# Optimization experiments

Hardware: AMD Instinct MI355X
Metric: run time of the kernel (lower is better)

Reference implementation:

```python
import jax, jax.numpy as jnp
import numpy as np
import math

D_MODEL = 1024
NUM_HEADS = 16
SEQ = 2048
BATCH = 4


def setup_inputs() -> dict:
    key = jax.random.key(0)
    ks = jax.random.split(key, 7)
    s = 0.02
    return {
        "x": jax.random.normal(ks[0], (BATCH, SEQ, D_MODEL), jnp.float32),
        "Wq": jax.random.normal(ks[1], (D_MODEL, D_MODEL), jnp.float32) * s,
        "bq": jax.random.normal(ks[2], (D_MODEL,), jnp.float32) * s,
        "Wkv": jax.random.normal(ks[3], (D_MODEL, 2 * D_MODEL), jnp.float32) * s,
        "bkv": jax.random.normal(ks[4], (2 * D_MODEL,), jnp.float32) * s,
        "Wo": jax.random.normal(ks[5], (D_MODEL, D_MODEL), jnp.float32) * s,
        "bo": jax.random.normal(ks[6], (D_MODEL,), jnp.float32) * s,
        "decoderMask": 1,
    }


def reference(x, Wq, bq, Wkv, bkv, Wo, bo, decoderMask):
    B, S, D = x.shape
    H = NUM_HEADS
    dh = D // H
    q_ = x @ Wq + bq              # [B,S,D]
    kv_ = x @ Wkv + bkv           # [B,S,2D] (self-attention: m is None)
    # Faithful to source: concat [q_, kv_] then reshape into heads of 3*dh,
    # which interleaves Q/KV projection columns across heads.
    qkv = jnp.concatenate([q_, kv_], axis=-1)          # [B,S,3D]
    qkv = qkv.reshape(B, S, H, 3 * dh).transpose(0, 2, 1, 3)  # [B,H,S,3dh]
    q, k, v = jnp.split(qkv, 3, axis=-1)               # each [B,H,S,dh]
    scaled = jnp.einsum("bhqd,bhkd->bhqk", q, k) / math.sqrt(dh)
    if decoderMask:
        mask = jnp.triu(jnp.full((S, S), -jnp.inf, dtype=scaled.dtype), k=1)
        scaled = scaled + mask
    attn = jax.nn.softmax(scaled, axis=-1)
    vals = jnp.einsum("bhqk,bhkd->bhqd", attn, v)      # [B,H,S,dh]
    vals = vals.transpose(0, 2, 1, 3).reshape(B, S, D)
    return vals @ Wo + bo
```

## Files before the change

kernel.cpp:

```cpp
#include <hip/hip_runtime.h>
#include <cstddef>
#include <cstdint>

#define SEQ   2048
#define BATCH 4
#define DM    1024
#define NH    16
#define DH    64
#define ROWS  (BATCH*SEQ)
#define NC3   3072
#define SM_SCALE 0.18033688f

typedef unsigned short u16;
typedef __attribute__((ext_vector_type(8))) short bf16x8;
typedef __attribute__((ext_vector_type(2))) float f32x2;
typedef __attribute__((ext_vector_type(4))) float f32x4;
typedef __attribute__((ext_vector_type(16))) float f32x16;
typedef __attribute__((ext_vector_type(4))) unsigned u32x4;
typedef __attribute__((ext_vector_type(2))) unsigned u32x2;

union V16 { f32x16 v; f32x2 p[8]; };

__device__ __forceinline__ u16 f2b(float f) {
  union { float f; unsigned u; } v; v.f = f;
  unsigned r = v.u + 0x7fffu + ((v.u >> 16) & 1u);
  return (u16)(r >> 16);
}

__device__ __forceinline__ unsigned cvt_pk_bf16(float lo, float hi) {
  unsigned r;
  asm("v_cvt_pk_bf16_f32 %0, %1, %2" : "=v"(r) : "v"(lo), "v"(hi));
  return r;
}

__device__ __forceinline__ void plswap(unsigned& a, unsigned& b) {
  auto rr = __builtin_amdgcn_permlane32_swap((int)a, (int)b, false, false);
  a = (unsigned)rr[0];
  b = (unsigned)rr[1];
}

__device__ __forceinline__ float ex2(float x) { return __builtin_amdgcn_exp2f(x); }

__device__ __forceinline__ void gld16(const void* g, void* l) {
  __builtin_amdgcn_global_load_lds((const __attribute__((address_space(1))) void*)g,
                                   (__attribute__((address_space(3))) void*)l,
                                   16, 0, 0);
}

__global__ __launch_bounds__(256) void prep_tw_kernel(
    const float* __restrict__ x, const float* __restrict__ bq,
    const float* __restrict__ bkv, u16* __restrict__ xb, float* __restrict__ bc,
    const float* __restrict__ Wq, const float* __restrict__ Wkv,
    const float* __restrict__ Wo, u16* __restrict__ Wt)
{
  __shared__ float t_[32][33];
  const int tid = threadIdx.x;
  if (blockIdx.x < 8192) {
    int i = blockIdx.x * 256 + tid;
    int idx = i * 4;
    float4 v = *(const float4*)(x + idx);
    u32x2 pv;
    pv[0] = cvt_pk_bf16(v.x, v.y);
    pv[1] = cvt_pk_bf16(v.z, v.w);
    *(u32x2*)&xb[idx] = pv;
    if (i < NC3) bc[i] = (i < DM) ? bq[i] : bkv[i - DM];
  } else {
    const int bid = blockIdx.x - 8192;
    const int n0 = (bid & 127) * 32, k0 = (bid >> 7) * 32;
    const int xcol = tid & 31, yrow = tid >> 5;
    #pragma unroll
    for (int it = 0; it < 4; ++it) {
      int k = k0 + yrow + it * 8;
      int n = n0 + xcol;
      float v;
      if (n < DM)           v = Wq[k * DM + n];
      else if (n < NC3)     v = Wkv[k * (2 * DM) + (n - DM)];
      else                  v = Wo[k * DM + (n - NC3)];
      t_[yrow + it * 8][xcol] = v;
    }
    __syncthreads();
    #pragma unroll
    for (int it = 0; it < 4; ++it) {
      int n = n0 + yrow + it * 8;
      int k = k0 + xcol;
      Wt[(size_t)n * DM + k] = f2b(t_[xcol][yrow + it * 8]);
    }
  }
}

__global__ __launch_bounds__(512, 2) void gemm8_qkv(
    const u16* __restrict__ A, const u16* __restrict__ Bt,
    const float* __restrict__ bias, u16* __restrict__ C, u16* __restrict__ Vt)
{
  constexpr int K = 1024, N = NC3;
  constexpr int ASLOT = 16384;
  constexpr int BBASE = 32768;
  constexpr int BSLOT = 12288;
  __shared__ alignas(16) u16 lds_[57344];

  const int tid = threadIdx.x;
  const int lane = tid & 63, wid = tid >> 6;
  const int wr2 = wid >> 2, wc4 = wid & 3;
  const int l15 = lane & 15, lhi = lane >> 4;

  const int bid = blockIdx.x;
  const int xcd = bid & 7, t = bid >> 3;
  const int row0 = (xcd * 4 + (t & 3)) * 256;
  const int hh   = t >> 2;
  const int col0 = hh * 192;

  const int sr = tid >> 3;
  const int scg = ((tid & 7) ^ (sr & 7)) * 8;
  const u16* aSrc = A  + (size_t)(row0 + sr) * K + scg;
  const u16* bSrc = Bt + (size_t)(col0 + sr) * K + scg;
  const int dLin = tid * 8;

  auto stA = [&](int kt, int u) {
    gld16(aSrc + (size_t)(u * 64) * K + kt * 64,
          lds_ + (kt & 1) * ASLOT + u * 4096 + dLin);
  };
  auto stB = [&](int kt, int u) {
    gld16(bSrc + (size_t)(u * 64) * K + kt * 64,
          lds_ + BBASE + (kt & 1) * BSLOT + u * 4096 + dLin);
  };

  int csw[2];
  csw[0] = ((lhi)     ^ (l15 & 7)) * 8;
  csw[1] = ((4 + lhi) ^ (l15 & 7)) * 8;
  const int aBase = wr2 * 8192 + l15 * 64;
  const int bBase = BBASE + (wc4 * 48 + l15) * 64;

  f32x4 acc[8][3];
  #pragma unroll
  for (int m = 0; m < 8; ++m)
    #pragma unroll
    for (int n = 0; n < 3; ++n) { f32x4 z = {0.f, 0.f, 0.f, 0.f}; acc[m][n] = z; }

  stA(0, 0); stA(0, 1); stA(0, 2); stA(0, 3);
  stB(0, 0); stB(0, 1); stB(0, 2);
  stB(1, 0); stB(1, 1); stB(1, 2);
  asm volatile("s_waitcnt vmcnt(3)" ::: "memory");
  __builtin_amdgcn_s_barrier();

  constexpr int KT2 = K / 128;
  for (int j = 0; j < KT2; ++j) {
    const bool last = (j == KT2 - 1);
    #pragma unroll
    for (int hk = 0; hk < 2; ++hk) {
      const int slotA = hk * ASLOT;
      const int slotB = hk * BSLOT;
      bf16x8 bfr[3][2];
      #pragma unroll
      for (int ph = 0; ph < 4; ++ph) {
        const int gp = hk * 4 + ph;
        if (ph == 0) {
          #pragma unroll
          for (int n = 0; n < 3; ++n)
            #pragma unroll
            for (int kk = 0; kk < 2; ++kk)
              bfr[n][kk] = *(const bf16x8*)&lds_[bBase + slotB + n * 1024 + csw[kk]];
        }
        bf16x8 af[2][2];
        #pragma unroll
        for (int mi = 0; mi < 2; ++mi)
          #pragma unroll
          for (int kk = 0; kk < 2; ++kk)
            af[mi][kk] = *(const bf16x8*)&lds_[aBase + slotA + (ph * 2 + mi) * 1024 + csw[kk]];
        switch (gp) {
          case 0: stA(2 * j + 1, 0); stA(2 * j + 1, 1); break;
          case 1: stA(2 * j + 1, 2); stA(2 * j + 1, 3); break;
          case 2: if (!last) { stB(2 * j + 2, 0); stB(2 * j + 2, 1); } break;
          case 3: if (!last) { stB(2 * j + 2, 2); } break;
          case 4: if (!last) { stA(2 * j + 2, 0); stA(2 * j + 2, 1); } break;
          case 5: if (!last) { stA(2 * j + 2, 2); stA(2 * j + 2, 3); } break;
          case 6: if (!last) { stB(2 * j + 3, 0); stB(2 * j + 3, 1); } break;
          case 7: if (!last) { stB(2 * j + 3, 2); } break;
        }
        __builtin_amdgcn_s_barrier();
        asm volatile("s_waitcnt lgkmcnt(0)" ::: "memory");
        __builtin_amdgcn_sched_barrier(0);
        __builtin_amdgcn_s_setprio(1);
        #pragma unroll
        for (int mi = 0; mi < 2; ++mi)
          #pragma unroll
          for (int n = 0; n < 3; ++n) {
            acc[ph * 2 + mi][n] =
                __builtin_amdgcn_mfma_f32_16x16x32_bf16(af[mi][0], bfr[n][0], acc[ph * 2 + mi][n], 0, 0, 0);
            acc[ph * 2 + mi][n] =
                __builtin_amdgcn_mfma_f32_16x16x32_bf16(af[mi][1], bfr[n][1], acc[ph * 2 + mi][n], 0, 0, 0);
          }
        __builtin_amdgcn_s_setprio(0);
        if (gp == 3) {
          if (last) { asm volatile("s_waitcnt vmcnt(0)" ::: "memory"); }
          else      { asm volatile("s_waitcnt vmcnt(3)" ::: "memory"); }
        } else if (gp == 7 && !last) {
          asm volatile("s_waitcnt vmcnt(3)" ::: "memory");
        }
        __builtin_amdgcn_s_barrier();
      }
    }
  }

  #pragma unroll
  for (int m = 0; m < 8; ++m) {
    const int row = row0 + wr2 * 128 + m * 16 + lhi * 4;
    #pragma unroll
    for (int n = 0; n < 3; ++n) {
      const int cc  = wc4 * 48 + n * 16 + l15;
      const int col = col0 + cc;
      const float bv = bias[col];
      if (cc < 128) {
        const float qs = (cc < 64) ? SM_SCALE : 1.f;
        #pragma unroll
        for (int r = 0; r < 4; ++r)
          C[(size_t)(row + r) * N + col] = f2b((acc[m][n][r] + bv) * qs);
      } else {
        u16 wv[4];
        #pragma unroll
        for (int r = 0; r < 4; ++r) wv[r] = f2b(acc[m][n][r] + bv);
        const int bb = row >> 11, jj = row & (SEQ - 1);
        u16* vt = Vt + ((size_t)(bb * NH + hh) * 64 + (cc - 128)) * SEQ + jj;
        u32x2 pv = { (unsigned)wv[0] | ((unsigned)wv[1] << 16),
                     (unsigned)wv[2] | ((unsigned)wv[3] << 16) };
        *(u32x2*)vt = pv;
      }
    }
  }
}

__global__ __launch_bounds__(512, 2) void gemm8_out(
    const u16* __restrict__ A, const u16* __restrict__ Bt,
    const float* __restrict__ bias, float* __restrict__ C)
{
  constexpr int K = 1024, N = DM;
  constexpr int ASLOT = 16384;
  constexpr int BBASE = 32768;
  constexpr int BSLOT = 8192;
  __shared__ alignas(16) u16 lds_[49152];

  const int tid = threadIdx.x;
  const int lane = tid & 63, wid = tid >> 6;
  const int wr2 = wid >> 2, wc4 = wid & 3;
  const int l15 = lane & 15, lhi = lane >> 4;

  const int bid = blockIdx.x;
  const int xcd = bid & 7, t = bid >> 3;
  const int row0 = (xcd * 4 + (t & 3)) * 256;
  const int col0 = (t >> 2) * 128;

  const int sr = tid >> 3;
  const int scg = ((tid & 7) ^ (sr & 7)) * 8;
  const u16* aSrc = A  + (size_t)(row0 + sr) * K + scg;
  const u16* bSrc = Bt + (size_t)(col0 + sr) * K + scg;
  const int dLin = tid * 8;

  auto stA = [&](int kt, int u) {
    gld16(aSrc + (size_t)(u * 64) * K + kt * 64,
          lds_ + (kt & 1) * ASLOT + u * 4096 + dLin);
  };
  auto stB = [&](int kt, int u) {
    gld16(bSrc + (size_t)(u * 64) * K + kt * 64,
          lds_ + BBASE + (kt & 1) * BSLOT + u * 4096 + dLin);
  };

  int csw[2];
  csw[0] = ((lhi)     ^ (l15 & 7)) * 8;
  csw[1] = ((4 + lhi) ^ (l15 & 7)) * 8;
  const int aBase = wr2 * 8192 + l15 * 64;
  const int bBase = BBASE + (wc4 * 32 + l15) * 64;

  f32x4 acc[8][2];
  #pragma unroll
  for (int m = 0; m < 8; ++m)
    #pragma unroll
    for (int n = 0; n < 2; ++n) { f32x4 z = {0.f, 0.f, 0.f, 0.f}; acc[m][n] = z; }

  stA(0, 0); stA(0, 1); stA(0, 2); stA(0, 3);
  stB(0, 0); stB(0, 1);
  stB(1, 0); stB(1, 1);
  asm volatile("s_waitcnt vmcnt(2)" ::: "memory");
  __builtin_amdgcn_s_barrier();

  constexpr int KT2 = K / 128;
  for (int j = 0; j < KT2; ++j) {
    const bool last = (j == KT2 - 1);
    #pragma unroll
    for (int hk = 0; hk < 2; ++hk) {
      const int slotA = hk * ASLOT;
      const int slotB = hk * BSLOT;
      bf16x8 bfr[2][2];
      #pragma unroll
      for (int ph = 0; ph < 4; ++ph) {
        const int gp = hk * 4 + ph;
        if (ph == 0) {
          #pragma unroll
          for (int n = 0; n < 2; ++n)
            #pragma unroll
            for (int kk = 0; kk < 2; ++kk)
              bfr[n][kk] = *(const bf16x8*)&lds_[bBase + slotB + n * 1024 + csw[kk]];
        }
        bf16x8 af[2][2];
        #pragma unroll
        for (int mi = 0; mi < 2; ++mi)
          #pragma unroll
          for (int kk = 0; kk < 2; ++kk)
            af[mi][kk] = *(const bf16x8*)&lds_[aBase + slotA + (ph * 2 + mi) * 1024 + csw[kk]];
        switch (gp) {
          case 0: stA(2 * j + 1, 0); stA(2 * j + 1, 1); break;
          case 1: stA(2 * j + 1, 2); stA(2 * j + 1, 3); break;
          case 2: if (!last) { stB(2 * j + 2, 0); stB(2 * j + 2, 1); } break;
          case 4: if (!last) { stA(2 * j + 2, 0); stA(2 * j + 2, 1); } break;
          case 5: if (!last) { stA(2 * j + 2, 2); stA(2 * j + 2, 3); } break;
          case 6: if (!last) { stB(2 * j + 3, 0); stB(2 * j + 3, 1); } break;
          default: break;
        }
        __builtin_amdgcn_s_barrier();
        asm volatile("s_waitcnt lgkmcnt(0)" ::: "memory");
        __builtin_amdgcn_sched_barrier(0);
        __builtin_amdgcn_s_setprio(1);
        #pragma unroll
        for (int mi = 0; mi < 2; ++mi)
          #pragma unroll
          for (int n = 0; n < 2; ++n) {
            acc[ph * 2 + mi][n] =
                __builtin_amdgcn_mfma_f32_16x16x32_bf16(af[mi][0], bfr[n][0], acc[ph * 2 + mi][n], 0, 0, 0);
            acc[ph * 2 + mi][n] =
                __builtin_amdgcn_mfma_f32_16x16x32_bf16(af[mi][1], bfr[n][1], acc[ph * 2 + mi][n], 0, 0, 0);
          }
        __builtin_amdgcn_s_setprio(0);
        if (gp == 3) {
          if (last) { asm volatile("s_waitcnt vmcnt(0)" ::: "memory"); }
          else      { asm volatile("s_waitcnt vmcnt(2)" ::: "memory"); }
        } else if (gp == 7 && !last) {
          asm volatile("s_waitcnt vmcnt(2)" ::: "memory");
        }
        __builtin_amdgcn_s_barrier();
      }
    }
  }

  #pragma unroll
  for (int m = 0; m < 8; ++m) {
    const int row = row0 + wr2 * 128 + m * 16 + lhi * 4;
    #pragma unroll
    for (int n = 0; n < 2; ++n) {
      const int col = col0 + wc4 * 32 + n * 16 + l15;
      const float bv = bias[col];
      #pragma unroll
      for (int r = 0; r < 4; ++r)
        C[(size_t)(row + r) * N + col] = acc[m][n][r] + bv;
    }
  }
}

__global__ __launch_bounds__(512, 4) void attn_kernel(
    const u16* __restrict__ qkv, const u16* __restrict__ Vt, u16* __restrict__ ctx)
{
  const int bid = blockIdx.x;
  const int p   = (bid >> 3) & 7;
  const int g   = (bid & 7) + ((bid >> 6) << 3);
  const int h   = g & 15, b = g >> 4;
  const int tid = threadIdx.x;
  const int lane = tid & 63;
  const int hf  = tid >> 8;
  const int wid = (tid >> 6) & 3;
  const int l31 = lane & 31, lhi5 = lane >> 5;

  __shared__ alignas(16) u16 smem_[2 * 16384];
  u16* const smem = smem_ + hf * 16384;

  const int qt  = hf ? (7 - p) : (8 + p);
  const int q0  = qt * 128;
  const int ntL = qt * 2 + 2;
  const int ntMax = (8 + p) * 2 + 2;

  const size_t kv_row = (size_t)(b * NH + h) * 64;
  const int st = tid & 255;
  const int sr = st >> 3, sck = st & 7;
  const int scks = sck ^ (sr & 7);

  const u16* kSrc0 = qkv + (size_t)(b * SEQ + sr) * NC3 + h * 192 + 64 + scks * 8;
  const u16* kSrc1 = kSrc0 + (size_t)32 * NC3;
  const u16* vSrc0 = Vt + (kv_row + sr) * SEQ + scks * 8;
  const u16* vSrc1 = vSrc0 + (size_t)32 * SEQ;
  const int dOff0 = sr * 64 + sck * 8;
  const int dOff1 = (32 + sr) * 64 + sck * 8;

  int koff[4], koff2[4];
  #pragma unroll
  for (int c = 0; c < 4; ++c) {
    koff[c]  = l31 * 64        + (((2 * c + lhi5) ^ (l31 & 7)) * 8);
    koff2[c] = (32 + l31) * 64 + (((2 * c + lhi5) ^ (l31 & 7)) * 8);
  }

  #pragma unroll
  for (int it = 0; it < 4; ++it) {
    int row = it * 32 + sr;
    gld16(qkv + (size_t)(b * SEQ + q0 + row) * NC3 + h * 192 + scks * 8,
          &smem[row * 64 + sck * 8]);
  }
  gld16(kSrc0, &smem[8192 + dOff0]);
  gld16(kSrc1, &smem[8192 + dOff1]);
  gld16(vSrc0, &smem[12288 + dOff0]);
  gld16(vSrc1, &smem[12288 + dOff1]);
  __syncthreads();

  bf16x8 qf[4];
  {
    const int qrow = wid * 32 + l31;
    #pragma unroll
    for (int c = 0; c < 4; ++c)
      qf[c] = *(const bf16x8*)&smem[qrow * 64 + (((2 * c + lhi5) ^ (qrow & 7)) * 8)];
  }
  __syncthreads();

  V16 o0, o1;
  #pragma unroll
  for (int r = 0; r < 16; ++r) { o0.v[r] = 0.f; o1.v[r] = 0.f; }
  float lrow = 0.f;

  const int qw0 = q0 + wid * 32;
  const int qa  = qw0 + l31;
  const int dqb = qa - 4 * lhi5;

  #pragma unroll 1
  for (int jt = 0; jt < ntMax; ++jt) {
    const int j0 = jt * 64;
    const u16* Kb = smem + ((jt & 1) ? 0 : 8192);
    const u16* Vb = smem + ((jt & 1) ? 4096 : 12288);

    if (jt + 1 < ntL) {
      u16* Kn = smem + ((jt & 1) ? 8192 : 0);
      u16* Vn = smem + ((jt & 1) ? 12288 : 4096);
      const size_t kAdv = (size_t)(j0 + 64) * NC3;
      const int    vAdv = j0 + 64;
      gld16(kSrc0 + kAdv, &Kn[dOff0]);
      gld16(kSrc1 + kAdv, &Kn[dOff1]);
      gld16(vSrc0 + vAdv, &Vn[dOff0]);
      gld16(vSrc1 + vAdv, &Vn[dOff1]);
    }

    if (j0 <= qw0 + 31) {
      V16 s0, s1;
      #pragma unroll
      for (int r = 0; r < 16; ++r) { s0.v[r] = 0.f; s1.v[r] = 0.f; }
      __builtin_amdgcn_s_setprio(1);
      #pragma unroll
      for (int c = 0; c < 4; ++c) {
        bf16x8 kf = *(const bf16x8*)&Kb[koff[c]];
        s0.v = __builtin_amdgcn_mfma_f32_32x32x16_bf16(kf, qf[c], s0.v, 0, 0, 0);
      }
      #pragma unroll
      for (int c = 0; c < 4; ++c) {
        bf16x8 kf = *(const bf16x8*)&Kb[koff2[c]];
        s1.v = __builtin_amdgcn_mfma_f32_32x32x16_bf16(kf, qf[c], s1.v, 0, 0, 0);
      }
      __builtin_amdgcn_s_setprio(0);

      if (j0 + 63 > qw0) {
        const int dq = dqb - j0;
        #pragma unroll
        for (int r = 0; r < 16; ++r) {
          const int kvc = (r & 3) + 8 * (r >> 2);
          s0.v[r] = (kvc > dq)      ? -1e30f : s0.v[r];
          s1.v[r] = (kvc + 32 > dq) ? -1e30f : s1.v[r];
        }
      }

      f32x2 sum2 = {0.f, 0.f};
      #pragma unroll
      for (int i = 0; i < 8; ++i) {
        f32x2 e0, e1;
        e0[0] = ex2(s0.p[i][0]); e0[1] = ex2(s0.p[i][1]);
        e1[0] = ex2(s1.p[i][0]); e1[1] = ex2(s1.p[i][1]);
        s0.p[i] = e0; s1.p[i] = e1;
        sum2 += e0 + e1;
      }
      float ps = sum2[0] + sum2[1];
      {
        unsigned a = __builtin_bit_cast(unsigned, ps), bb = a;
        plswap(a, bb);
        ps = __builtin_bit_cast(float, a) + __builtin_bit_cast(float, bb);
      }
      lrow += ps;

      unsigned pk0[8], pk1[8];
      #pragma unroll
      for (int i = 0; i < 4; ++i) {
        pk0[2 * i]     = cvt_pk_bf16(s0.v[4 * i + 0], s0.v[4 * i + 1]);
        pk0[2 * i + 1] = cvt_pk_bf16(s0.v[4 * i + 2], s0.v[4 * i + 3]);
        pk1[2 * i]     = cvt_pk_bf16(s1.v[4 * i + 0], s1.v[4 * i + 1]);
        pk1[2 * i + 1] = cvt_pk_bf16(s1.v[4 * i + 2], s1.v[4 * i + 3]);
      }
      bf16x8 pf[4];
      {
        unsigned a0 = pk0[0], b0 = pk0[2]; plswap(a0, b0);
        unsigned a1 = pk0[1], b1 = pk0[3]; plswap(a1, b1);
        u32x4 w0v = {a0, a1, b0, b1}; pf[0] = __builtin_bit_cast(bf16x8, w0v);
        unsigned a2 = pk0[4], b2 = pk0[6]; plswap(a2, b2);
        unsigned a3 = pk0[5], b3 = pk0[7]; plswap(a3, b3);
        u32x4 w1v = {a2, a3, b2, b3}; pf[1] = __builtin_bit_cast(bf16x8, w1v);
        unsigned a4 = pk1[0], b4 = pk1[2]; plswap(a4, b4);
        unsigned a5 = pk1[1], b5 = pk1[3]; plswap(a5, b5);
        u32x4 w2v = {a4, a5, b4, b5}; pf[2] = __builtin_bit_cast(bf16x8, w2v);
        unsigned a6 = pk1[4], b6 = pk1[6]; plswap(a6, b6);
        unsigned a7 = pk1[5], b7 = pk1[7]; plswap(a7, b7);
        u32x4 w3v = {a6, a7, b6, b7}; pf[3] = __builtin_bit_cast(bf16x8, w3v);
      }

      __builtin_amdgcn_s_setprio(1);
      #pragma unroll
      for (int c = 0; c < 4; ++c) {
        bf16x8 vf = *(const bf16x8*)&Vb[koff[c]];
        o0.v = __builtin_amdgcn_mfma_f32_32x32x16_bf16(vf, pf[c], o0.v, 0, 0, 0);
      }
      #pragma unroll
      for (int c = 0; c < 4; ++c) {
        bf16x8 vf = *(const bf16x8*)&Vb[koff2[c]];
        o1.v = __builtin_amdgcn_mfma_f32_32x32x16_bf16(vf, pf[c], o1.v, 0, 0, 0);
      }
      __builtin_amdgcn_s_setprio(0);
    }
    __syncthreads();
  }

  const float inv = 1.f / lrow;
  u16* crow = ctx + (size_t)(b * SEQ + qa) * DM + h * DH;
  #pragma unroll
  for (int i = 0; i < 4; ++i) {
    u32x2 v0, v1;
    v0[0] = cvt_pk_bf16(o0.v[4 * i + 0] * inv, o0.v[4 * i + 1] * inv);
    v0[1] = cvt_pk_bf16(o0.v[4 * i + 2] * inv, o0.v[4 * i + 3] * inv);
    v1[0] = cvt_pk_bf16(o1.v[4 * i + 0] * inv, o1.v[4 * i + 1] * inv);
    v1[1] = cvt_pk_bf16(o1.v[4 * i + 2] * inv, o1.v[4 * i + 3] * inv);
    *(u32x2*)&crow[8 * i + 4 * lhi5]      = v0;
    *(u32x2*)&crow[32 + 8 * i + 4 * lhi5] = v1;
  }
}

extern "C" void kernel_launch(void* const* d_in, const int* in_sizes, int n_in,
                              void* d_out, int out_size, void* d_ws, size_t ws_size,
                              hipStream_t stream) {
  (void)in_sizes; (void)n_in; (void)out_size; (void)ws_size;
  const float* x   = (const float*)d_in[0];
  const float* Wq  = (const float*)d_in[1];
  const float* bq  = (const float*)d_in[2];
  const float* Wkv = (const float*)d_in[3];
  const float* bkv = (const float*)d_in[4];
  const float* Wo  = (const float*)d_in[5];
  const float* bo  = (const float*)d_in[6];
  float* out = (float*)d_out;

  char* w = (char*)d_ws;
  size_t off = 0;
  auto alloc = [&](size_t bytes) { void* p = w + off; off += (bytes + 255) & ~(size_t)255; return p; };
  u16*   xb   = (u16*)alloc((size_t)ROWS * DM * 2);
  u16*   qkvb = (u16*)alloc((size_t)ROWS * NC3 * 2);
  u16*   Vt   = (u16*)alloc((size_t)BATCH * NH * DH * SEQ * 2);
  u16*   Wt   = (u16*)alloc((size_t)4096 * DM * 2);
  float* bc   = (float*)alloc((size_t)NC3 * 4);
  u16*   ctx  = xb;

  prep_tw_kernel<<<dim3(8192 + 4096), 256, 0, stream>>>(x, bq, bkv, xb, bc, Wq, Wkv, Wo, Wt);
  gemm8_qkv<<<dim3(512), 512, 0, stream>>>(xb, Wt, bc, qkvb, Vt);
  attn_kernel<<<dim3(512), 512, 0, stream>>>(qkvb, Vt, ctx);
  gemm8_out<<<dim3(256), 512, 0, stream>>>(ctx, Wt + (size_t)NC3 * DM, bo, out);
}
```

Before: 153.9 us.

## Split heavy query tile's KV range across both block halves with LDS merge

Each attention block now balances work between its two 256-thread halves. Half 0 processes the heavy query tile over its first KV tiles. Half 1 finishes its own light tile, then takes over the remaining KV tiles of the heavy tile, and the two partial accumulators and row sums are merged through shared memory. Shared memory grows to 80KB and launch bounds drop to 2 blocks per SM, which lowers potential occupancy in exchange for equal 17-iteration loops per half.

Result: faster. 149.6 us (median of 3 runs) (-2.8%).

```diff
diff --git a/kernel.cpp b/kernel.cpp
--- a/kernel.cpp
+++ b/kernel.cpp
@@ -353,7 +353,7 @@
   }
 }
 
-__global__ __launch_bounds__(512, 4) void attn_kernel(
+__global__ __launch_bounds__(512, 2) void attn_kernel(
     const u16* __restrict__ qkv, const u16* __restrict__ Vt, u16* __restrict__ ctx)
 {
   const int bid = blockIdx.x;
@@ -363,16 +363,16 @@
   const int tid = threadIdx.x;
   const int lane = tid & 63;
   const int hf  = tid >> 8;
-  const int wid = (tid >> 6) & 3;
+  const int wid2 = (tid >> 6) & 3;
   const int l31 = lane & 31, lhi5 = lane >> 5;
 
-  __shared__ alignas(16) u16 smem_[2 * 16384];
-  u16* const smem = smem_ + hf * 16384;
-
-  const int qt  = hf ? (7 - p) : (8 + p);
-  const int q0  = qt * 128;
-  const int ntL = qt * 2 + 2;
-  const int ntMax = (8 + p) * 2 + 2;
+  __shared__ alignas(16) u16 smem[40960];
+  u16* const AQ = smem;
+  u16* const KV = smem + 8192 + hf * 16384;
+
+  const int bTiles = 16 - 2 * p;
+  const int qtA = 8 + p;
+  const int qtSelf = hf ? (7 - p) : qtA;
 
   const size_t kv_row = (size_t)(b * NH + h) * 64;
   const int st = tid & 255;
@@ -386,6 +386,15 @@
   const int dOff0 = sr * 64 + sck * 8;
   const int dOff1 = (32 + sr) * 64 + sck * 8;
 
+  auto stageKV = [&](int jt, u16* buf) {
+    const size_t kAdv = (size_t)(jt * 64) * NC3;
+    const int    vAdv = jt * 64;
+    gld16(kSrc0 + kAdv, buf + dOff0);
+    gld16(kSrc1 + kAdv, buf + dOff1);
+    gld16(vSrc0 + vAdv, buf + 4096 + dOff0);
+    gld16(vSrc1 + vAdv, buf + 4096 + dOff1);
+  };
+
   int koff[4], koff2[4];
   #pragma unroll
   for (int c = 0; c < 4; ++c) {
@@ -393,24 +402,26 @@
     koff2[c] = (32 + l31) * 64 + (((2 * c + lhi5) ^ (l31 & 7)) * 8);
   }
 
-  #pragma unroll
-  for (int it = 0; it < 4; ++it) {
-    int row = it * 32 + sr;
-    gld16(qkv + (size_t)(b * SEQ + q0 + row) * NC3 + h * 192 + scks * 8,
-          &smem[row * 64 + sck * 8]);
-  }
-  gld16(kSrc0, &smem[8192 + dOff0]);
-  gld16(kSrc1, &smem[8192 + dOff1]);
-  gld16(vSrc0, &smem[12288 + dOff0]);
-  gld16(vSrc1, &smem[12288 + dOff1]);
+  {
+    const int q0S = qtSelf * 128;
+    u16* const QDST = hf ? KV : AQ;
+    #pragma unroll
+    for (int it = 0; it < 4; ++it) {
+      int row = it * 32 + sr;
+      gld16(qkv + (size_t)(b * SEQ + q0S + row) * NC3 + h * 192 + scks * 8,
+            QDST + row * 64 + sck * 8);
+    }
+    stageKV(0, KV + 8192);
+  }
   __syncthreads();
 
   bf16x8 qf[4];
   {
-    const int qrow = wid * 32 + l31;
+    const int qrow = wid2 * 32 + l31;
+    const u16* qsrc = hf ? KV : AQ;
     #pragma unroll
     for (int c = 0; c < 4; ++c)
-      qf[c] = *(const bf16x8*)&smem[qrow * 64 + (((2 * c + lhi5) ^ (qrow & 7)) * 8)];
+      qf[c] = *(const bf16x8*)&qsrc[qrow * 64 + (((2 * c + lhi5) ^ (qrow & 7)) * 8)];
   }
   __syncthreads();
 
@@ -419,25 +430,50 @@
   for (int r = 0; r < 16; ++r) { o0.v[r] = 0.f; o1.v[r] = 0.f; }
   float lrow = 0.f;
 
-  const int qw0 = q0 + wid * 32;
-  const int qa  = qw0 + l31;
-  const int dqb = qa - 4 * lhi5;
+  int q0  = qtSelf * 128;
+  int qw0 = q0 + wid2 * 32;
+  int qa  = qw0 + l31;
+  int dqb = qa - 4 * lhi5;
+
+  auto storeOut = [&]() {
+    const float inv = 1.f / lrow;
+    u16* crow = ctx + (size_t)(b * SEQ + qa) * DM + h * DH;
+    #pragma unroll
+    for (int i = 0; i < 4; ++i) {
+      u32x2 v0, v1;
+      v0[0] = cvt_pk_bf16(o0.v[4 * i + 0] * inv, o0.v[4 * i + 1] * inv);
+      v0[1] = cvt_pk_bf16(o0.v[4 * i + 2] * inv, o0.v[4 * i + 3] * inv);
+      v1[0] = cvt_pk_bf16(o1.v[4 * i + 0] * inv, o1.v[4 * i + 1] * inv);
+      v1[1] = cvt_pk_bf16(o1.v[4 * i + 2] * inv, o1.v[4 * i + 3] * inv);
+      *(u32x2*)&crow[8 * i + 4 * lhi5]      = v0;
+      *(u32x2*)&crow[32 + 8 * i + 4 * lhi5] = v1;
+    }
+  };
 
   #pragma unroll 1
-  for (int jt = 0; jt < ntMax; ++jt) {
+  for (int it = 0; it < 17; ++it) {
+    if (hf == 1 && it == bTiles) {
+      storeOut();
+      #pragma unroll
+      for (int r = 0; r < 16; ++r) { o0.v[r] = 0.f; o1.v[r] = 0.f; }
+      lrow = 0.f;
+      q0 = qtA * 128; qw0 = q0 + wid2 * 32; qa = qw0 + l31; dqb = qa - 4 * lhi5;
+      const int qrow = wid2 * 32 + l31;
+      #pragma unroll
+      for (int c = 0; c < 4; ++c)
+        qf[c] = *(const bf16x8*)&AQ[qrow * 64 + (((2 * c + lhi5) ^ (qrow & 7)) * 8)];
+    }
+
+    const int jt = (hf == 0) ? it : (it < bTiles ? it : 17 + (it - bTiles));
     const int j0 = jt * 64;
-    const u16* Kb = smem + ((jt & 1) ? 0 : 8192);
-    const u16* Vb = smem + ((jt & 1) ? 4096 : 12288);
-
-    if (jt + 1 < ntL) {
-      u16* Kn = smem + ((jt & 1) ? 8192 : 0);
-      u16* Vn = smem + ((jt & 1) ? 12288 : 4096);
-      const size_t kAdv = (size_t)(j0 + 64) * NC3;
-      const int    vAdv = j0 + 64;
-      gld16(kSrc0 + kAdv, &Kn[dOff0]);
-      gld16(kSrc1 + kAdv, &Kn[dOff1]);
-      gld16(vSrc0 + vAdv, &Vn[dOff0]);
-      gld16(vSrc1 + vAdv, &Vn[dOff1]);
+    const u16* buf = KV + ((it + 1) & 1) * 8192;
+    const u16* Kb = buf;
+    const u16* Vb = buf + 4096;
+
+    if (it + 1 < 17) {
+      const int itN = it + 1;
+      const int jtN = (hf == 0) ? itN : (itN < bTiles ? itN : 17 + (itN - bTiles));
+      stageKV(jtN, KV + (it & 1) * 8192);
     }
 
     if (j0 <= qw0 + 31) {
@@ -524,17 +560,21 @@
     __syncthreads();
   }
 
-  const float inv = 1.f / lrow;
-  u16* crow = ctx + (size_t)(b * SEQ + qa) * DM + h * DH;
-  #pragma unroll
-  for (int i = 0; i < 4; ++i) {
-    u32x2 v0, v1;
-    v0[0] = cvt_pk_bf16(o0.v[4 * i + 0] * inv, o0.v[4 * i + 1] * inv);
-    v0[1] = cvt_pk_bf16(o0.v[4 * i + 2] * inv, o0.v[4 * i + 3] * inv);
-    v1[0] = cvt_pk_bf16(o1.v[4 * i + 0] * inv, o1.v[4 * i + 1] * inv);
-    v1[1] = cvt_pk_bf16(o1.v[4 * i + 2] * inv, o1.v[4 * i + 3] * inv);
-    *(u32x2*)&crow[8 * i + 4 * lhi5]      = v0;
-    *(u32x2*)&crow[32 + 8 * i + 4 * lhi5] = v1;
+  float* const poA = (float*)(smem + 8192);
+  float* const plA = (float*)smem;
+  if (hf == 1) {
+    const int base2 = st * 32;
+    #pragma unroll
+    for (int i = 0; i < 16; ++i) { poA[base2 + i] = o0.v[i]; poA[base2 + 16 + i] = o1.v[i]; }
+    plA[st] = lrow;
+  }
+  __syncthreads();
+  if (hf == 0) {
+    const int base2 = st * 32;
+    #pragma unroll
+    for (int i = 0; i < 16; ++i) { o0.v[i] += poA[base2 + i]; o1.v[i] += poA[base2 + 16 + i]; }
+    lrow += plA[st];
+    storeOut();
   }
 }
 
```
